# Kernel optimization log

Hardware: AMD Instinct MI355X
Metric: run time of the kernel (lower is better)

The kernel has to match this reference:

```python
import jax, jax.numpy as jnp
import numpy as np

N_NODES = 50000
N_EDGES = 600000
N_GRAPHS = 512
D = 128          # in_channels == hidden_channels
L = 4            # num_layers (total GINConv count)
N_CLASSES = 10
BN_EPS = 1e-5


def setup_inputs() -> dict:
    key = jax.random.key(0)
    ks = jax.random.split(key, 12)
    x = jax.random.normal(ks[0], (N_NODES, D), dtype=jnp.float32)
    edge_index = jax.random.randint(ks[1], (2, N_EDGES), 0, N_NODES, dtype=jnp.int64)
    batch = jnp.sort(jax.random.randint(ks[2], (N_NODES,), 0, N_GRAPHS, dtype=jnp.int64))
    s = 1.0 / np.sqrt(D)
    W1 = jax.random.uniform(ks[3], (L, D, D), jnp.float32, -s, s)
    b1 = jax.random.uniform(ks[4], (L, D), jnp.float32, -s, s)
    W2 = jax.random.uniform(ks[5], (L, D, D), jnp.float32, -s, s)
    b2 = jax.random.uniform(ks[6], (L, D), jnp.float32, -s, s)
    eps = jnp.zeros((L,), jnp.float32)            # train_eps=True, init 0
    gamma = jnp.ones((L, D), jnp.float32)
    beta = jnp.zeros((L, D), jnp.float32)
    sl = 1.0 / np.sqrt(D * L)
    Wlin = jax.random.uniform(ks[7], (D * L, N_CLASSES), jnp.float32, -sl, sl)
    blin = jax.random.uniform(ks[8], (N_CLASSES,), jnp.float32, -sl, sl)
    return {"x": x, "edge_index": edge_index, "batch": batch,
            "W1": W1, "b1": b1, "W2": W2, "b2": b2, "eps": eps,
            "gamma": gamma, "beta": beta, "Wlin": Wlin, "blin": blin}


def reference(x, edge_index, batch, W1, b1, W2, b2, eps, gamma, beta, Wlin, blin):
    src, dst = edge_index[0], edge_index[1]
    h = x
    pools = []
    for l in range(L):
        # GINConv: sum-aggregate neighbor features at dst, add (1+eps)*self
        agg = jax.ops.segment_sum(h[src], dst, num_segments=N_NODES)
        z = (1.0 + eps[l]) * h + agg
        # 2-layer MLP
        z = jnp.maximum(z @ W1[l] + b1[l], 0.0) @ W2[l] + b2[l]
        # BatchNorm1d (training mode: batch stats, biased variance)
        mean = jnp.mean(z, axis=0)
        var = jnp.mean(jnp.square(z - mean), axis=0)
        z = (z - mean) * jax.lax.rsqrt(var + BN_EPS) * gamma[l] + beta[l]
        h = jnp.maximum(z, 0.0)
        # global_add_pool per graph
        pools.append(jax.ops.segment_sum(h, batch, num_segments=N_GRAPHS))
    x_cat = jnp.concatenate(pools, axis=1)  # [N_GRAPHS, D*L]
    return x_cat @ Wlin + blin              # dropout = identity (eval)
```

## Files before the change

kernel.cpp:

```cpp
#include <hip/hip_runtime.h>

#define N_NODES 50000
#define N_EDGES 600000
#define N_GRAPHS 512
#define DIM 128
#define NLAYERS 4
#define NCLASSES 10
#define KPS 136

typedef __attribute__((ext_vector_type(8))) short short8;
typedef __attribute__((ext_vector_type(4))) float f32x4;

union Frag { short8 s; uint4 u; };

__device__ inline unsigned short f2bf(float v) {
    union { float f; unsigned u; } c; c.f = v;
    unsigned u = c.u;
    u += 0x7FFFu + ((u >> 16) & 1u);
    return (unsigned short)(u >> 16);
}
__device__ inline float bfu_lo(unsigned u) {
    union { float f; unsigned x; } c; c.x = u << 16; return c.f;
}
__device__ inline float bfu_hi(unsigned u) {
    union { float f; unsigned x; } c; c.x = u & 0xFFFF0000u; return c.f;
}
__device__ inline void addRow(float* acc, const uint4& v) {
    acc[0] += bfu_lo(v.x); acc[1] += bfu_hi(v.x);
    acc[2] += bfu_lo(v.y); acc[3] += bfu_hi(v.y);
    acc[4] += bfu_lo(v.z); acc[5] += bfu_hi(v.z);
    acc[6] += bfu_lo(v.w); acc[7] += bfu_hi(v.w);
}

__global__ __launch_bounds__(256) void hist_kernel(
    const int* __restrict__ dst, int* __restrict__ deg)
{
    int e = blockIdx.x * 256 + threadIdx.x;
    if (e >= N_EDGES) return;
    atomicAdd(&deg[dst[e]], 1);
}

__global__ __launch_bounds__(256) void scan1_kernel(
    const int* __restrict__ deg, int* __restrict__ bsum)
{
    __shared__ int red[256];
    int t = threadIdx.x;
    int i4 = blockIdx.x * 256 + t;
    int s = 0;
    if (i4 < 12500) {
        int4 v = ((const int4*)deg)[i4];
        s = v.x + v.y + v.z + v.w;
    }
    red[t] = s;
    __syncthreads();
    for (int off = 128; off > 0; off >>= 1) {
        if (t < off) red[t] += red[t + off];
        __syncthreads();
    }
    if (t == 0) bsum[blockIdx.x] = red[0];
}

__global__ __launch_bounds__(64) void scan2_kernel(int* __restrict__ bsum,
                                                   int* __restrict__ dbins)
{
    __shared__ int sh[64];
    int t = threadIdx.x;
    dbins[t] = 0;
    sh[t] = (t < 49) ? bsum[t] : 0;
    __syncthreads();
    if (t == 0) {
        int run = 0;
        for (int i = 0; i < 49; i++) { int v = sh[i]; sh[i] = run; run += v; }
    }
    __syncthreads();
    if (t < 49) bsum[t] = sh[t];
}

__global__ __launch_bounds__(256) void scan3_kernel(
    const int* __restrict__ deg, const int* __restrict__ bsum,
    int* __restrict__ rowptr, int* __restrict__ cursor,
    int* __restrict__ dbins)
{
    __shared__ int red[256];
    __shared__ int lh[64];
    int t = threadIdx.x;
    int i4 = blockIdx.x * 256 + t;
    int4 v = {0, 0, 0, 0};
    if (i4 < 12500) v = ((const int4*)deg)[i4];
    int s = v.x + v.y + v.z + v.w;
    red[t] = s;
    __syncthreads();
    for (int off = 1; off < 256; off <<= 1) {
        int val = (t >= off) ? red[t - off] : 0;
        __syncthreads();
        red[t] += val;
        __syncthreads();
    }
    int run = bsum[blockIdx.x] + (t ? red[t - 1] : 0);
    if (i4 < 12500) {
        int4 rp;
        rp.x = run; run += v.x;
        rp.y = run; run += v.y;
        rp.z = run; run += v.z;
        rp.w = run; run += v.w;
        ((int4*)rowptr)[i4] = rp;
        ((int4*)cursor)[i4] = rp;
    }
    if (blockIdx.x == 0 && t == 0) rowptr[N_NODES] = N_EDGES;

    if (t < 64) lh[t] = 0;
    __syncthreads();
    if (i4 < 12500) {
        atomicAdd(&lh[min(v.x, 63)], 1);
        atomicAdd(&lh[min(v.y, 63)], 1);
        atomicAdd(&lh[min(v.z, 63)], 1);
        atomicAdd(&lh[min(v.w, 63)], 1);
    }
    __syncthreads();
    if (t < 64 && lh[t]) atomicAdd(&dbins[t], lh[t]);
}

__global__ __launch_bounds__(64) void dscan_kernel(
    const int* __restrict__ dbins, int* __restrict__ dcur)
{
    if (threadIdx.x == 0) {
        int run = 0;
        for (int i = 0; i < 64; i++) { dcur[i] = run; run += dbins[i]; }
    }
}

__global__ __launch_bounds__(256) void dperm_kernel(
    const int* __restrict__ rowptr, int* __restrict__ dcur,
    int* __restrict__ perm)
{
    __shared__ int lh[64];
    int t = threadIdx.x;
    int n = blockIdx.x * 256 + t;
    bool valid = (n < N_NODES);
    int b = 0, r = 0;
    if (t < 64) lh[t] = 0;
    __syncthreads();
    if (valid) {
        int d = rowptr[n + 1] - rowptr[n];
        b = min(d, 63);
        r = atomicAdd(&lh[b], 1);
    }
    __syncthreads();
    if (t < 64) lh[t] = atomicAdd(&dcur[t], lh[t]);
    __syncthreads();
    if (valid) perm[lh[b] + r] = n;
}

__global__ __launch_bounds__(256) void fill_kernel(
    const int* __restrict__ src, const int* __restrict__ dst,
    int* __restrict__ cursor, int* __restrict__ csr)
{
    int e = blockIdx.x * 256 + threadIdx.x;
    if (e >= N_EDGES) return;
    int p = atomicAdd(&cursor[dst[e]], 1);
    csr[p] = src[e];
}

__global__ __launch_bounds__(256) void prep_kernel(
    const int* __restrict__ batch, int* __restrict__ gstart,
    const float* __restrict__ x, unsigned int* __restrict__ xb,
    const float* __restrict__ W1, const float* __restrict__ W2,
    unsigned short* __restrict__ whi, float* __restrict__ stats)
{
    int b = blockIdx.x;
    int t = threadIdx.x;
    if (b < 196) {
        int n = b * 256 + t;
        if (n >= N_NODES) return;
        int bb = batch[n];
        int bp = (n == 0) ? -1 : batch[n - 1];
        for (int g = bp + 1; g <= bb; g++) gstart[g] = n;
        if (n == N_NODES - 1)
            for (int g = bb + 1; g <= N_GRAPHS; g++) gstart[g] = N_NODES;
    } else if (b < 6446) {
        int idx = (b - 196) * 256 + t;
        if (idx >= N_NODES * 32) return;
        float4 v = ((const float4*)x)[idx];
        uint2 o;
        o.x = (unsigned)f2bf(v.x) | ((unsigned)f2bf(v.y) << 16);
        o.y = (unsigned)f2bf(v.z) | ((unsigned)f2bf(v.w) << 16);
        ((uint2*)xb)[idx] = o;
    } else if (b < 6958) {
        int idx = (b - 6446) * 256 + t;
        int f   = idx & 16383;
        int w01 = (idx >> 14) & 1;
        int l   = idx >> 15;
        int j    = f & 7;
        int lane = (f >> 3) & 63;
        int cg   = (f >> 9) & 7;
        int ks   = f >> 12;
        int k = ks * 32 + (lane >> 4) * 8 + j;
        int n = cg * 16 + (lane & 15);
        const float* W = (w01 == 0 ? W1 : W2) + (size_t)l * 16384;
        whi[idx] = f2bf(W[k * 128 + n]);
    } else {
        #pragma unroll
        for (int i = 0; i < 4; i++) stats[i * 256 + t] = 0.f;
    }
}

__global__ __launch_bounds__(256) void gin_layer_kernel(
    const unsigned int* __restrict__ hb,
    const int* __restrict__ rowptr, const int* __restrict__ csr,
    const int* __restrict__ perm,
    const float* __restrict__ epsP,
    unsigned short* __restrict__ z,
    const unsigned short* __restrict__ whi,
    const float* __restrict__ b1, const float* __restrict__ b2,
    float* __restrict__ stats)
{
    __shared__ unsigned short tpk[64 * KPS];
    __shared__ float sums[1024];
    __shared__ float sqs[1024];

    const int t = threadIdx.x;
    const int lane = t & 63;
    const int w = t >> 6;
    const int wr = w & 1, wc = w >> 1;
    const int l15 = lane & 15, quad = lane >> 4;
    const int base = blockIdx.x * 64;

    {
        const int m = t >> 2;
        const int c = t & 3;
        const int idx = base + m;
        const int n = (idx < N_NODES) ? perm[idx] : N_NODES;
        const uint4* hb4 = (const uint4*)hb;
        float acc[32];
        #pragma unroll
        for (int i = 0; i < 32; i++) acc[i] = 0.f;
        if (n < N_NODES) {
            const float e1 = 1.0f + epsP[0];
            const uint4* self = hb4 + (size_t)n * 16 + c;
            #pragma unroll
            for (int j = 0; j < 4; j++) {
                uint4 v = self[j * 4];
                float* a = acc + j * 8;
                a[0] = e1 * bfu_lo(v.x); a[1] = e1 * bfu_hi(v.x);
                a[2] = e1 * bfu_lo(v.y); a[3] = e1 * bfu_hi(v.y);
                a[4] = e1 * bfu_lo(v.z); a[5] = e1 * bfu_hi(v.z);
                a[6] = e1 * bfu_lo(v.w); a[7] = e1 * bfu_hi(v.w);
            }
            int beg = rowptr[n], end = rowptr[n + 1];
            int e = beg;
            if (e + 3 < end) {
                int s0 = csr[e], s1 = csr[e + 1], s2 = csr[e + 2], s3 = csr[e + 3];
                while (true) {
                    const uint4* r0 = hb4 + (size_t)s0 * 16 + c;
                    const uint4* r1 = hb4 + (size_t)s1 * 16 + c;
                    const uint4* r2 = hb4 + (size_t)s2 * 16 + c;
                    const uint4* r3 = hb4 + (size_t)s3 * 16 + c;
                    uint4 v00 = r0[0], v01 = r0[4], v02 = r0[8], v03 = r0[12];
                    uint4 v10 = r1[0], v11 = r1[4], v12 = r1[8], v13 = r1[12];
                    uint4 v20 = r2[0], v21 = r2[4], v22 = r2[8], v23 = r2[12];
                    uint4 v30 = r3[0], v31 = r3[4], v32 = r3[8], v33 = r3[12];
                    int en = e + 4;
                    bool more = (en + 3 < end);
                    if (more) {
                        s0 = csr[en]; s1 = csr[en + 1];
                        s2 = csr[en + 2]; s3 = csr[en + 3];
                    }
                    addRow(acc + 0, v00); addRow(acc + 8, v01); addRow(acc + 16, v02); addRow(acc + 24, v03);
                    addRow(acc + 0, v10); addRow(acc + 8, v11); addRow(acc + 16, v12); addRow(acc + 24, v13);
                    addRow(acc + 0, v20); addRow(acc + 8, v21); addRow(acc + 16, v22); addRow(acc + 24, v23);
                    addRow(acc + 0, v30); addRow(acc + 8, v31); addRow(acc + 16, v32); addRow(acc + 24, v33);
                    e = en;
                    if (!more) break;
                }
            }
            for (; e < end; e++) {
                int s0 = csr[e];
                const uint4* r0 = hb4 + (size_t)s0 * 16 + c;
                uint4 a0 = r0[0], a1 = r0[4], a2 = r0[8], a3 = r0[12];
                addRow(acc + 0, a0);  addRow(acc + 8, a1);
                addRow(acc + 16, a2); addRow(acc + 24, a3);
            }
        }
        #pragma unroll
        for (int j = 0; j < 4; j++) {
            union { short8 s; unsigned short u[8]; } pk;
            #pragma unroll
            for (int i = 0; i < 8; i++) pk.u[i] = f2bf(acc[j * 8 + i]);
            *((short8*)&tpk[m * KPS + j * 32 + c * 8]) = pk.s;
        }
    }
    __syncthreads();

    f32x4 acc[2][4];
    #pragma unroll
    for (int s = 0; s < 2; s++)
        #pragma unroll
        for (int i = 0; i < 4; i++) acc[s][i] = (f32x4){0.f, 0.f, 0.f, 0.f};

    const int arow0 = (32 * wr + l15) * KPS;
    const int arow1 = arow0 + 16 * KPS;

    #pragma unroll
    for (int kh = 0; kh < 2; kh++) {
        Frag bf[2][4];
        short8 a0[2], a1[2];
        #pragma unroll
        for (int kk = 0; kk < 2; kk++) {
            int ks = kh * 2 + kk;
            #pragma unroll
            for (int i = 0; i < 4; i++) {
                size_t woff = (size_t)(((ks * 8 + wc * 4 + i) * 64 + lane) * 8);
                bf[kk][i].s = *((const short8*)&whi[woff]);
            }
            a0[kk] = *((const short8*)&tpk[arow0 + ks * 32 + quad * 8]);
            a1[kk] = *((const short8*)&tpk[arow1 + ks * 32 + quad * 8]);
        }
        #pragma unroll
        for (int kk = 0; kk < 2; kk++) {
            #pragma unroll
            for (int i = 0; i < 4; i++) {
                acc[0][i] = __builtin_amdgcn_mfma_f32_16x16x32_bf16(a0[kk], bf[kk][i].s, acc[0][i], 0, 0, 0);
                acc[1][i] = __builtin_amdgcn_mfma_f32_16x16x32_bf16(a1[kk], bf[kk][i].s, acc[1][i], 0, 0, 0);
            }
        }
    }
    __syncthreads();

    #pragma unroll
    for (int i = 0; i < 4; i++) {
        int col = wc * 64 + i * 16 + l15;
        float bb = b1[col];
        #pragma unroll
        for (int s = 0; s < 2; s++) {
            #pragma unroll
            for (int r = 0; r < 4; r++) {
                int m = 32 * wr + 16 * s + quad * 4 + r;
                float v = fmaxf(acc[s][i][r] + bb, 0.f);
                tpk[m * KPS + col] = f2bf(v);
            }
            acc[s][i] = (f32x4){0.f, 0.f, 0.f, 0.f};
        }
    }
    __syncthreads();

    const unsigned short* w2 = whi + 16384;
    #pragma unroll
    for (int kh = 0; kh < 2; kh++) {
        Frag bf[2][4];
        short8 a0[2], a1[2];
        #pragma unroll
        for (int kk = 0; kk < 2; kk++) {
            int ks = kh * 2 + kk;
            #pragma unroll
            for (int i = 0; i < 4; i++) {
                size_t woff = (size_t)(((ks * 8 + wc * 4 + i) * 64 + lane) * 8);
                bf[kk][i].s = *((const short8*)&w2[woff]);
            }
            a0[kk] = *((const short8*)&tpk[arow0 + ks * 32 + quad * 8]);
            a1[kk] = *((const short8*)&tpk[arow1 + ks * 32 + quad * 8]);
        }
        #pragma unroll
        for (int kk = 0; kk < 2; kk++) {
            #pragma unroll
            for (int i = 0; i < 4; i++) {
                acc[0][i] = __builtin_amdgcn_mfma_f32_16x16x32_bf16(a0[kk], bf[kk][i].s, acc[0][i], 0, 0, 0);
                acc[1][i] = __builtin_amdgcn_mfma_f32_16x16x32_bf16(a1[kk], bf[kk][i].s, acc[1][i], 0, 0, 0);
            }
        }
    }
    __syncthreads();

    {
        float colsum[4], colsq[4];
        #pragma unroll
        for (int i = 0; i < 4; i++) {
            int col = wc * 64 + i * 16 + l15;
            float bb = b2[col];
            float su = 0.f, q2 = 0.f;
            #pragma unroll
            for (int s = 0; s < 2; s++) {
                #pragma unroll
                for (int r = 0; r < 4; r++) {
                    int m = 32 * wr + 16 * s + quad * 4 + r;
                    int n = base + m;
                    float v = acc[s][i][r] + bb;
                    tpk[m * KPS + col] = f2bf(v);
                    if (n < N_NODES) { su += v; q2 += v * v; }
                }
            }
            colsum[i] = su; colsq[i] = q2;
        }
        #pragma unroll
        for (int i = 0; i < 4; i++) {
            sums[(w * 4 + i) * 64 + lane] = colsum[i];
            sqs [(w * 4 + i) * 64 + lane] = colsq[i];
        }
    }
    __syncthreads();

    {
        int m2 = t >> 2, c2 = t & 3;
        int idx2 = base + m2;
        if (idx2 < N_NODES) {
            int n2 = perm[idx2];
            const uint4* srcp = (const uint4*)(tpk + m2 * KPS);
            uint4* dstp = (uint4*)z + (size_t)n2 * 16;
            #pragma unroll
            for (int j = 0; j < 4; j++) dstp[j * 4 + c2] = srcp[j * 4 + c2];
        }
    }
    if (t < 128) {
        int c = t;
        int wcc = c >> 6, ci = (c >> 4) & 3, cl = c & 15;
        float s = 0.f, q2 = 0.f;
        #pragma unroll
        for (int wrr = 0; wrr < 2; wrr++) {
            int ww = wcc * 2 + wrr;
            #pragma unroll
            for (int u = 0; u < 4; u++) {
                int ln = cl + u * 16;
                s  += sums[(ww * 4 + ci) * 64 + ln];
                q2 += sqs [(ww * 4 + ci) * 64 + ln];
            }
        }
        unsafeAtomicAdd(&stats[c], s);
        unsafeAtomicAdd(&stats[128 + c], q2);
    }
}

__global__ __launch_bounds__(256) void bnpool_kernel(
    const unsigned int* __restrict__ z, const float* __restrict__ stats,
    const float* __restrict__ gamma, const float* __restrict__ beta,
    const int* __restrict__ gstart, unsigned int* __restrict__ hout,
    float* __restrict__ pools, int layer)
{
    __shared__ float red[8][128];
    const int g = blockIdx.x;
    const int t = threadIdx.x;
    const int q = t & 31, r = t >> 5;
    const int beg = gstart[g], end = gstart[g + 1];

    float4 s  = ((const float4*)stats)[q];
    float4 sq = ((const float4*)stats)[32 + q];
    float4 gm = ((const float4*)gamma)[q];
    float4 bt = ((const float4*)beta)[q];
    const float invN = 1.0f / (float)N_NODES;
    float m, vr;
    float4 scl, sh;
    m = s.x * invN; vr = sq.x * invN - m * m; scl.x = gm.x * rsqrtf(vr + 1e-5f); sh.x = bt.x - m * scl.x;
    m = s.y * invN; vr = sq.y * invN - m * m; scl.y = gm.y * rsqrtf(vr + 1e-5f); sh.y = bt.y - m * scl.y;
    m = s.z * invN; vr = sq.z * invN - m * m; scl.z = gm.z * rsqrtf(vr + 1e-5f); sh.z = bt.z - m * scl.z;
    m = s.w * invN; vr = sq.w * invN - m * m; scl.w = gm.w * rsqrtf(vr + 1e-5f); sh.w = bt.w - m * scl.w;

    float4 acc = {0.f, 0.f, 0.f, 0.f};
    for (int n = beg + r; n < end; n += 8) {
        uint2 zp = ((const uint2*)z)[(size_t)n * 32 + q];
        float4 hv;
        hv.x = fmaxf(bfu_lo(zp.x) * scl.x + sh.x, 0.f);
        hv.y = fmaxf(bfu_hi(zp.x) * scl.y + sh.y, 0.f);
        hv.z = fmaxf(bfu_lo(zp.y) * scl.z + sh.z, 0.f);
        hv.w = fmaxf(bfu_hi(zp.y) * scl.w + sh.w, 0.f);
        uint2 p;
        p.x = (unsigned)f2bf(hv.x) | ((unsigned)f2bf(hv.y) << 16);
        p.y = (unsigned)f2bf(hv.z) | ((unsigned)f2bf(hv.w) << 16);
        ((uint2*)hout)[(size_t)n * 32 + q] = p;
        acc.x += hv.x; acc.y += hv.y; acc.z += hv.z; acc.w += hv.w;
    }
    red[r][q * 4 + 0] = acc.x;
    red[r][q * 4 + 1] = acc.y;
    red[r][q * 4 + 2] = acc.z;
    red[r][q * 4 + 3] = acc.w;
    __syncthreads();
    if (t < 128) {
        float sm = 0.f;
        #pragma unroll
        for (int rr = 0; rr < 8; rr++) sm += red[rr][t];
        pools[(size_t)g * (DIM * NLAYERS) + (size_t)layer * DIM + t] = sm;
    }
}

__global__ __launch_bounds__(256) void bnhead_kernel(
    const unsigned int* __restrict__ z, const float* __restrict__ stats,
    const float* __restrict__ gamma, const float* __restrict__ beta,
    const int* __restrict__ gstart, const float* __restrict__ pools,
    const float* __restrict__ Wlin, const float* __restrict__ blin,
    float* __restrict__ out)
{
    __shared__ float red[8][128];
    __shared__ float pool3[128];
    const int g = blockIdx.x;
    const int t = threadIdx.x;
    const int q = t & 31, r = t >> 5;
    const int beg = gstart[g], end = gstart[g + 1];

    float4 s  = ((const float4*)stats)[q];
    float4 sq = ((const float4*)stats)[32 + q];
    float4 gm = ((const float4*)gamma)[q];
    float4 bt = ((const float4*)beta)[q];
    const float invN = 1.0f / (float)N_NODES;
    float m, vr;
    float4 scl, sh;
    m = s.x * invN; vr = sq.x * invN - m * m; scl.x = gm.x * rsqrtf(vr + 1e-5f); sh.x = bt.x - m * scl.x;
    m = s.y * invN; vr = sq.y * invN - m * m; scl.y = gm.y * rsqrtf(vr + 1e-5f); sh.y = bt.y - m * scl.y;
    m = s.z * invN; vr = sq.z * invN - m * m; scl.z = gm.z * rsqrtf(vr + 1e-5f); sh.z = bt.z - m * scl.z;
    m = s.w * invN; vr = sq.w * invN - m * m; scl.w = gm.w * rsqrtf(vr + 1e-5f); sh.w = bt.w - m * scl.w;

    float4 acc = {0.f, 0.f, 0.f, 0.f};
    for (int n = beg + r; n < end; n += 8) {
        uint2 zp = ((const uint2*)z)[(size_t)n * 32 + q];
        acc.x += fmaxf(bfu_lo(zp.x) * scl.x + sh.x, 0.f);
        acc.y += fmaxf(bfu_hi(zp.x) * scl.y + sh.y, 0.f);
        acc.z += fmaxf(bfu_lo(zp.y) * scl.z + sh.z, 0.f);
        acc.w += fmaxf(bfu_hi(zp.y) * scl.w + sh.w, 0.f);
    }
    red[r][q * 4 + 0] = acc.x;
    red[r][q * 4 + 1] = acc.y;
    red[r][q * 4 + 2] = acc.z;
    red[r][q * 4 + 3] = acc.w;
    __syncthreads();
    if (t < 128) {
        float sm = 0.f;
        #pragma unroll
        for (int rr = 0; rr < 8; rr++) sm += red[rr][t];
        pool3[t] = sm;
    }
    __syncthreads();

    if (t < 64) {
        const int lane = t;
        const float* xr = pools + (size_t)g * (DIM * NLAYERS);
        float a[NCLASSES];
        #pragma unroll
        for (int o = 0; o < NCLASSES; o++) a[o] = 0.f;
        #pragma unroll
        for (int kk = 0; kk < DIM * NLAYERS; kk += 64) {
            float xv = (kk < 3 * DIM) ? xr[kk + lane] : pool3[kk - 3 * DIM + lane];
            const float* wrow = Wlin + (size_t)(kk + lane) * NCLASSES;
            #pragma unroll
            for (int o = 0; o < NCLASSES; o++) a[o] += xv * wrow[o];
        }
        #pragma unroll
        for (int o = 0; o < NCLASSES; o++) {
            float v = a[o];
            #pragma unroll
            for (int off = 32; off > 0; off >>= 1) v += __shfl_down(v, off, 64);
            if (lane == 0) out[(size_t)g * NCLASSES + o] = v + blin[o];
        }
    }
}

extern "C" void kernel_launch(void* const* d_in, const int* in_sizes, int n_in,
                              void* d_out, int out_size, void* d_ws, size_t ws_size,
                              hipStream_t stream)
{
    const float* x     = (const float*)d_in[0];
    const int*   src   = (const int*)d_in[1];
    const int*   dst   = ((const int*)d_in[1]) + N_EDGES;
    const int*   batch = (const int*)d_in[2];
    const float* W1    = (const float*)d_in[3];
    const float* b1    = (const float*)d_in[4];
    const float* W2    = (const float*)d_in[5];
    const float* b2    = (const float*)d_in[6];
    const float* eps   = (const float*)d_in[7];
    const float* gamma = (const float*)d_in[8];
    const float* beta  = (const float*)d_in[9];
    const float* Wlin  = (const float*)d_in[10];
    const float* blin  = (const float*)d_in[11];
    float* out = (float*)d_out;

    char* ws = (char*)d_ws;
    const size_t FEATH = (size_t)N_NODES * DIM * sizeof(unsigned short);
    size_t off = 0;
    unsigned int* buf_h = (unsigned int*)(ws + off); off += FEATH;
    unsigned short* buf_z = (unsigned short*)(ws + off); off += FEATH;
    float* pools  = (float*)(ws + off); off += (size_t)N_GRAPHS * DIM * NLAYERS * sizeof(float);
    float* stats  = (float*)(ws + off); off += (size_t)NLAYERS * 256 * sizeof(float);
    int*   deg    = (int*)(ws + off);   off += (size_t)N_NODES * sizeof(int);
    int*   rowptr = (int*)(ws + off);   off += (size_t)(N_NODES + 1) * sizeof(int) + 12;
    int*   csr    = (int*)(ws + off);   off += (size_t)N_EDGES * sizeof(int);
    int*   gstart = (int*)(ws + off);   off += 2064;
    int*   bsum   = (int*)(ws + off);   off += 208;
    unsigned short* whi = (unsigned short*)(ws + off); off += (size_t)NLAYERS * 2 * 16384 * 2;
    int*   dbins  = (int*)(ws + off);   off += 256;
    int*   dcur   = (int*)(ws + off);   off += 256;
    int*   perm   = (int*)(ws + off);   off += (size_t)N_NODES * sizeof(int);

    hipMemsetAsync(deg, 0, (size_t)N_NODES * sizeof(int), stream);

    hist_kernel<<<(N_EDGES + 255) / 256, 256, 0, stream>>>(dst, deg);
    scan1_kernel<<<49, 256, 0, stream>>>(deg, bsum);
    scan2_kernel<<<1, 64, 0, stream>>>(bsum, dbins);
    scan3_kernel<<<49, 256, 0, stream>>>(deg, bsum, rowptr, deg , dbins);
    fill_kernel<<<(N_EDGES + 255) / 256, 256, 0, stream>>>(src, dst, deg, csr);
    dscan_kernel<<<1, 64, 0, stream>>>(dbins, dcur);
    dperm_kernel<<<196, 256, 0, stream>>>(rowptr, dcur, perm);
    prep_kernel<<<6959, 256, 0, stream>>>(batch, gstart, x, buf_h,
                                          W1, W2, whi, stats);

    for (int l = 0; l < NLAYERS; l++) {
        gin_layer_kernel<<<(N_NODES + 63) / 64, 256, 0, stream>>>(
            buf_h, rowptr, csr, perm, eps + l, buf_z,
            whi + (size_t)l * 32768,
            b1 + (size_t)l * DIM, b2 + (size_t)l * DIM,
            stats + (size_t)l * 256);
        if (l < NLAYERS - 1) {
            bnpool_kernel<<<N_GRAPHS, 256, 0, stream>>>(
                (const unsigned int*)buf_z, stats + (size_t)l * 256,
                gamma + (size_t)l * DIM, beta + (size_t)l * DIM,
                gstart, buf_h, pools, l);
        }
    }
    bnhead_kernel<<<N_GRAPHS, 256, 0, stream>>>(
        (const unsigned int*)buf_z, stats + (size_t)(NLAYERS - 1) * 256,
        gamma + (size_t)(NLAYERS - 1) * DIM, beta + (size_t)(NLAYERS - 1) * DIM,
        gstart, pools, Wlin, blin, out);
}
```

Measured before the change: 398.8 us.

## Drop degree-sorted node permutation and deepen neighbor gather unroll to eight

Removes the degree-bucket histogram, scan and permutation kernels, so each GIN layer block processes nodes in natural order. This saves three small launches and the indirect perm lookups, but gives up the load balancing that grouping similar-degree nodes into one block provided. The neighbor aggregation loop now issues eight rows of gathers per iteration, with a four-row tail, to keep more loads in flight. A launch bound of three blocks per CU is added, which may restrict registers given the larger unroll.

```diff
diff --git a/kernel.cpp b/kernel.cpp
--- a/kernel.cpp
+++ b/kernel.cpp
@@ -60,12 +60,10 @@
     if (t == 0) bsum[blockIdx.x] = red[0];
 }
 
-__global__ __launch_bounds__(64) void scan2_kernel(int* __restrict__ bsum,
-                                                   int* __restrict__ dbins)
+__global__ __launch_bounds__(64) void scan2_kernel(int* __restrict__ bsum)
 {
     __shared__ int sh[64];
     int t = threadIdx.x;
-    dbins[t] = 0;
     sh[t] = (t < 49) ? bsum[t] : 0;
     __syncthreads();
     if (t == 0) {
@@ -78,11 +76,9 @@
 
 __global__ __launch_bounds__(256) void scan3_kernel(
     const int* __restrict__ deg, const int* __restrict__ bsum,
-    int* __restrict__ rowptr, int* __restrict__ cursor,
-    int* __restrict__ dbins)
+    int* __restrict__ rowptr, int* __restrict__ cursor)
 {
     __shared__ int red[256];
-    __shared__ int lh[64];
     int t = threadIdx.x;
     int i4 = blockIdx.x * 256 + t;
     int4 v = {0, 0, 0, 0};
@@ -107,48 +103,6 @@
         ((int4*)cursor)[i4] = rp;
     }
     if (blockIdx.x == 0 && t == 0) rowptr[N_NODES] = N_EDGES;
-
-    if (t < 64) lh[t] = 0;
-    __syncthreads();
-    if (i4 < 12500) {
-        atomicAdd(&lh[min(v.x, 63)], 1);
-        atomicAdd(&lh[min(v.y, 63)], 1);
-        atomicAdd(&lh[min(v.z, 63)], 1);
-        atomicAdd(&lh[min(v.w, 63)], 1);
-    }
-    __syncthreads();
-    if (t < 64 && lh[t]) atomicAdd(&dbins[t], lh[t]);
-}
-
-__global__ __launch_bounds__(64) void dscan_kernel(
-    const int* __restrict__ dbins, int* __restrict__ dcur)
-{
-    if (threadIdx.x == 0) {
-        int run = 0;
-        for (int i = 0; i < 64; i++) { dcur[i] = run; run += dbins[i]; }
-    }
-}
-
-__global__ __launch_bounds__(256) void dperm_kernel(
-    const int* __restrict__ rowptr, int* __restrict__ dcur,
-    int* __restrict__ perm)
-{
-    __shared__ int lh[64];
-    int t = threadIdx.x;
-    int n = blockIdx.x * 256 + t;
-    bool valid = (n < N_NODES);
-    int b = 0, r = 0;
-    if (t < 64) lh[t] = 0;
-    __syncthreads();
-    if (valid) {
-        int d = rowptr[n + 1] - rowptr[n];
-        b = min(d, 63);
-        r = atomicAdd(&lh[b], 1);
-    }
-    __syncthreads();
-    if (t < 64) lh[t] = atomicAdd(&dcur[t], lh[t]);
-    __syncthreads();
-    if (valid) perm[lh[b] + r] = n;
 }
 
 __global__ __launch_bounds__(256) void fill_kernel(
@@ -204,10 +158,9 @@
     }
 }
 
-__global__ __launch_bounds__(256) void gin_layer_kernel(
+__global__ __launch_bounds__(256, 3) void gin_layer_kernel(
     const unsigned int* __restrict__ hb,
     const int* __restrict__ rowptr, const int* __restrict__ csr,
-    const int* __restrict__ perm,
     const float* __restrict__ epsP,
     unsigned short* __restrict__ z,
     const unsigned short* __restrict__ whi,
@@ -228,8 +181,7 @@
     {
         const int m = t >> 2;
         const int c = t & 3;
-        const int idx = base + m;
-        const int n = (idx < N_NODES) ? perm[idx] : N_NODES;
+        const int n = base + m;
         const uint4* hb4 = (const uint4*)hb;
         float acc[32];
         #pragma unroll
@@ -248,30 +200,59 @@
             }
             int beg = rowptr[n], end = rowptr[n + 1];
             int e = beg;
-            if (e + 3 < end) {
-                int s0 = csr[e], s1 = csr[e + 1], s2 = csr[e + 2], s3 = csr[e + 3];
+            if (e + 7 < end) {
+                int s0 = csr[e],     s1 = csr[e + 1], s2 = csr[e + 2], s3 = csr[e + 3];
+                int s4 = csr[e + 4], s5 = csr[e + 5], s6 = csr[e + 6], s7 = csr[e + 7];
                 while (true) {
                     const uint4* r0 = hb4 + (size_t)s0 * 16 + c;
                     const uint4* r1 = hb4 + (size_t)s1 * 16 + c;
                     const uint4* r2 = hb4 + (size_t)s2 * 16 + c;
                     const uint4* r3 = hb4 + (size_t)s3 * 16 + c;
+                    const uint4* r4 = hb4 + (size_t)s4 * 16 + c;
+                    const uint4* r5 = hb4 + (size_t)s5 * 16 + c;
+                    const uint4* r6 = hb4 + (size_t)s6 * 16 + c;
+                    const uint4* r7 = hb4 + (size_t)s7 * 16 + c;
                     uint4 v00 = r0[0], v01 = r0[4], v02 = r0[8], v03 = r0[12];
                     uint4 v10 = r1[0], v11 = r1[4], v12 = r1[8], v13 = r1[12];
                     uint4 v20 = r2[0], v21 = r2[4], v22 = r2[8], v23 = r2[12];
                     uint4 v30 = r3[0], v31 = r3[4], v32 = r3[8], v33 = r3[12];
-                    int en = e + 4;
-                    bool more = (en + 3 < end);
+                    uint4 v40 = r4[0], v41 = r4[4], v42 = r4[8], v43 = r4[12];
+                    uint4 v50 = r5[0], v51 = r5[4], v52 = r5[8], v53 = r5[12];
+                    uint4 v60 = r6[0], v61 = r6[4], v62 = r6[8], v63 = r6[12];
+                    uint4 v70 = r7[0], v71 = r7[4], v72 = r7[8], v73 = r7[12];
+                    int en = e + 8;
+                    bool more = (en + 7 < end);
                     if (more) {
-                        s0 = csr[en]; s1 = csr[en + 1];
-                        s2 = csr[en + 2]; s3 = csr[en + 3];
+                        s0 = csr[en];     s1 = csr[en + 1]; s2 = csr[en + 2]; s3 = csr[en + 3];
+                        s4 = csr[en + 4]; s5 = csr[en + 5]; s6 = csr[en + 6]; s7 = csr[en + 7];
                     }
                     addRow(acc + 0, v00); addRow(acc + 8, v01); addRow(acc + 16, v02); addRow(acc + 24, v03);
                     addRow(acc + 0, v10); addRow(acc + 8, v11); addRow(acc + 16, v12); addRow(acc + 24, v13);
                     addRow(acc + 0, v20); addRow(acc + 8, v21); addRow(acc + 16, v22); addRow(acc + 24, v23);
                     addRow(acc + 0, v30); addRow(acc + 8, v31); addRow(acc + 16, v32); addRow(acc + 24, v33);
+                    addRow(acc + 0, v40); addRow(acc + 8, v41); addRow(acc + 16, v42); addRow(acc + 24, v43);
+                    addRow(acc + 0, v50); addRow(acc + 8, v51); addRow(acc + 16, v52); addRow(acc + 24, v53);
+                    addRow(acc + 0, v60); addRow(acc + 8, v61); addRow(acc + 16, v62); addRow(acc + 24, v63);
+                    addRow(acc + 0, v70); addRow(acc + 8, v71); addRow(acc + 16, v72); addRow(acc + 24, v73);
                     e = en;
                     if (!more) break;
                 }
+            }
+            if (e + 3 < end) {
+                int s0 = csr[e], s1 = csr[e + 1], s2 = csr[e + 2], s3 = csr[e + 3];
+                const uint4* r0 = hb4 + (size_t)s0 * 16 + c;
+                const uint4* r1 = hb4 + (size_t)s1 * 16 + c;
+                const uint4* r2 = hb4 + (size_t)s2 * 16 + c;
+                const uint4* r3 = hb4 + (size_t)s3 * 16 + c;
+                uint4 v00 = r0[0], v01 = r0[4], v02 = r0[8], v03 = r0[12];
+                uint4 v10 = r1[0], v11 = r1[4], v12 = r1[8], v13 = r1[12];
+                uint4 v20 = r2[0], v21 = r2[4], v22 = r2[8], v23 = r2[12];
+                uint4 v30 = r3[0], v31 = r3[4], v32 = r3[8], v33 = r3[12];
+                addRow(acc + 0, v00); addRow(acc + 8, v01); addRow(acc + 16, v02); addRow(acc + 24, v03);
+                addRow(acc + 0, v10); addRow(acc + 8, v11); addRow(acc + 16, v12); addRow(acc + 24, v13);
+                addRow(acc + 0, v20); addRow(acc + 8, v21); addRow(acc + 16, v22); addRow(acc + 24, v23);
+                addRow(acc + 0, v30); addRow(acc + 8, v31); addRow(acc + 16, v32); addRow(acc + 24, v33);
+                e += 4;
             }
             for (; e < end; e++) {
                 int s0 = csr[e];
@@ -400,9 +381,8 @@
 
     {
         int m2 = t >> 2, c2 = t & 3;
-        int idx2 = base + m2;
-        if (idx2 < N_NODES) {
-            int n2 = perm[idx2];
+        int n2 = base + m2;
+        if (n2 < N_NODES) {
             const uint4* srcp = (const uint4*)(tpk + m2 * KPS);
             uint4* dstp = (uint4*)z + (size_t)n2 * 16;
             #pragma unroll
@@ -581,25 +561,20 @@
     int*   gstart = (int*)(ws + off);   off += 2064;
     int*   bsum   = (int*)(ws + off);   off += 208;
     unsigned short* whi = (unsigned short*)(ws + off); off += (size_t)NLAYERS * 2 * 16384 * 2;
-    int*   dbins  = (int*)(ws + off);   off += 256;
-    int*   dcur   = (int*)(ws + off);   off += 256;
-    int*   perm   = (int*)(ws + off);   off += (size_t)N_NODES * sizeof(int);
 
     hipMemsetAsync(deg, 0, (size_t)N_NODES * sizeof(int), stream);
 
     hist_kernel<<<(N_EDGES + 255) / 256, 256, 0, stream>>>(dst, deg);
     scan1_kernel<<<49, 256, 0, stream>>>(deg, bsum);
-    scan2_kernel<<<1, 64, 0, stream>>>(bsum, dbins);
-    scan3_kernel<<<49, 256, 0, stream>>>(deg, bsum, rowptr, deg , dbins);
+    scan2_kernel<<<1, 64, 0, stream>>>(bsum);
+    scan3_kernel<<<49, 256, 0, stream>>>(deg, bsum, rowptr, deg );
     fill_kernel<<<(N_EDGES + 255) / 256, 256, 0, stream>>>(src, dst, deg, csr);
-    dscan_kernel<<<1, 64, 0, stream>>>(dbins, dcur);
-    dperm_kernel<<<196, 256, 0, stream>>>(rowptr, dcur, perm);
     prep_kernel<<<6959, 256, 0, stream>>>(batch, gstart, x, buf_h,
                                           W1, W2, whi, stats);
 
     for (int l = 0; l < NLAYERS; l++) {
         gin_layer_kernel<<<(N_NODES + 63) / 64, 256, 0, stream>>>(
-            buf_h, rowptr, csr, perm, eps + l, buf_z,
+            buf_h, rowptr, csr, eps + l, buf_z,
             whi + (size_t)l * 32768,
             b1 + (size_t)l * DIM, b2 + (size_t)l * DIM,
             stats + (size_t)l * 256);
```

Result: slower. 759.0 us (+90.3%).
